# Kernel tuning notes

Measured on AMD Instinct MI355X. Metric: run time of the kernel, lower is better.

Reference implementation:

```python
import jax, jax.numpy as jnp
import numpy as np

PAD = 1
ORDERS = ['back', 'down', 'front', 'left', 'right', 'top']
# connected face for each of ['up','down','left','right'] sides (from self.relation)
NEIGHBORS = {
    'back':  ['top', 'down', 'right', 'left'],
    'down':  ['front', 'back', 'left', 'right'],
    'front': ['top', 'down', 'left', 'right'],
    'left':  ['top', 'down', 'back', 'front'],
    'right': ['top', 'down', 'front', 'back'],
    'top':   ['back', 'front', 'left', 'right'],
}
SIDES = ['up', 'down', 'left', 'right']

def _rot_y(t):
    c, s = np.cos(t), np.sin(t)
    return np.array([[c, 0, s], [0, 1, 0], [-s, 0, c]], np.float64)

def _rot_x(t):
    c, s = np.cos(t), np.sin(t)
    return np.array([[1, 0, 0], [0, c, -s], [0, s, c]], np.float64)

def _precompute(h, pad):
    # Reconstruction of Equirec2Cube geometry used by SpherePad._GetLoc.
    # Padded cube face has side Wp = h + 2*pad and FOV theta = 2*arctan((0.5h+pad)/(0.5h)).
    Wp = h + 2 * pad
    cxp = (Wp - 1) / 2.0
    tan_half = (0.5 * h + pad) / (0.5 * h)  # tan(theta/2)
    fp = cxp / tan_half                      # focal of padded cube (pixel-edge convention)
    u = (np.arange(Wp) - cxp) / fp
    gx, gy = np.meshgrid(u, u)              # x right, y down, camera looks along +z
    grid = np.stack([gx, gy, np.ones_like(gx)], axis=-1)  # [Wp, Wp, 3] front-face rays
    # world->camera rotations per face, ordered/named to match ORDERS
    R = {'back': _rot_y(np.pi), 'down': _rot_x(np.pi / 2), 'front': np.eye(3),
         'left': _rot_y(np.pi / 2), 'right': _rot_y(-np.pi / 2), 'top': _rot_x(-np.pi / 2)}
    data = {}
    for face in ORDERS:
        data[face] = {}
        for j, side in enumerate(SIDES):
            conn = NEIGHBORS[face][j]
            Rrel = R[conn] @ R[face].T       # self-cam -> connected-cam
            g = grid @ Rrel.T                # [Wp, Wp, 3]
            # original FOV=90 K has f == cx, so normalized grid_sample coord = X/Z, Y/Z
            x = g[..., 0] / g[..., 2]
            y = g[..., 1] / g[..., 2]
            mask = (x >= -1.01) & (x <= 1.01) & (y >= -1.01) & (y <= 1.01)
            xy = np.clip(np.stack([x, y], axis=-1), -1.0, 1.0).astype(np.float32)
            if side == 'up':
                sl = (slice(0, pad), slice(None))
            elif side == 'down':
                sl = (slice(Wp - pad, Wp), slice(None))
            elif side == 'left':
                sl = (slice(None), slice(0, pad))
            else:
                sl = (slice(None), slice(Wp - pad, Wp))
            data[face][side] = (xy[sl], mask[sl])
    return data

def _grid_sample(img, grid):
    # img [N,C,H,W], grid [N,Hg,Wg,2] in [-1,1]; bilinear, align_corners=True
    N, C, H, W = img.shape
    x = (grid[..., 0] + 1.0) * 0.5 * (W - 1)
    y = (grid[..., 1] + 1.0) * 0.5 * (H - 1)
    x0 = jnp.floor(x)
    y0 = jnp.floor(y)
    wx = (x - x0)[..., None]
    wy = (y - y0)[..., None]
    x0i = jnp.clip(x0.astype(jnp.int32), 0, W - 1)
    x1i = jnp.clip(x0i + 1, 0, W - 1)
    y0i = jnp.clip(y0.astype(jnp.int32), 0, H - 1)
    y1i = jnp.clip(y0i + 1, 0, H - 1)
    b = jnp.arange(N)[:, None, None]
    v00 = img[b, :, y0i, x0i]  # [N,Hg,Wg,C]
    v01 = img[b, :, y0i, x1i]
    v10 = img[b, :, y1i, x0i]
    v11 = img[b, :, y1i, x1i]
    out = (v00 * (1 - wx) * (1 - wy) + v01 * wx * (1 - wy)
           + v10 * (1 - wx) * wy + v11 * wx * wy)
    return out.transpose(0, 3, 1, 2)  # [N,C,Hg,Wg]

def _forward(inputs, pad):
    bs, c, h, w = inputs.shape
    rep = bs // 6
    data = _precompute(h, pad)       # numpy constants, computed at trace time
    faces = inputs.reshape(rep, 6, c, h, w)   # inputs[i::6] == faces[:, i]
    outs = []
    for i, face in enumerate(ORDERS):
        tf = jnp.pad(faces[:, i], ((0, 0), (0, 0), (pad, pad), (pad, pad)))
        for j, side in enumerate(SIDES):
            conn = faces[:, ORDERS.index(NEIGHBORS[face][j])]
            xy, mask = data[face][side]
            grid = jnp.broadcast_to(jnp.asarray(xy), (rep,) + xy.shape)
            interp = _grid_sample(conn, grid)          # [rep,c,strip_h,strip_w]
            m = jnp.asarray(mask)[None, None]
            if side == 'up':
                tf = tf.at[:, :, :pad, :].set(jnp.where(m, interp, tf[:, :, :pad, :]))
            elif side == 'down':
                tf = tf.at[:, :, -pad:, :].set(jnp.where(m, interp, tf[:, :, -pad:, :]))
            elif side == 'left':
                tf = tf.at[:, :, :, :pad].set(jnp.where(m, interp, tf[:, :, :, :pad]))
            else:
                tf = tf.at[:, :, :, -pad:].set(jnp.where(m, interp, tf[:, :, :, -pad:]))
        outs.append(tf)
    # torch: cat by face then re-interleave -> out[k*6+i] = face i of panorama k
    return jnp.stack(outs, axis=1).reshape(bs, c, h + 2 * pad, w + 2 * pad)

def setup_inputs() -> dict:
    key = jax.random.key(0)
    inputs = jax.random.normal(key, (24, 256, 128, 128), dtype=jnp.float32)
    return {'inputs': inputs}

def reference(inputs):
    return _forward(inputs, PAD)
```

## Files before the change

### kernel.cpp

```cpp
#include <hip/hip_runtime.h>

#define H    128
#define WP   130
#define BPF  516
#define TBLN 3096
#define SPI  1536

__constant__ int c_R[6][9] = {
  {-1,0,0,  0,1,0,  0,0,-1},
  { 1,0,0,  0,0,-1, 0,1,0 },
  { 1,0,0,  0,1,0,  0,0,1 },
  { 0,0,1,  0,1,0, -1,0,0 },
  { 0,0,-1, 0,1,0,  1,0,0 },
  { 1,0,0,  0,0,1,  0,-1,0},
};
__constant__ int c_conn[6][4] = {
  {5,1,4,3}, {2,0,3,4}, {5,1,3,4}, {5,1,0,2}, {5,1,2,0}, {0,2,3,4},
};

#define INV_FP (65.0f / 4128.0f)

__device__ __forceinline__ int stage_index(int y, int x) {
  if (x <= 3)   return 512 + y * 8 + x;
  if (x >= 124) return 512 + y * 8 + 4 + (x - 124);
  int slot = (y == 0) ? 0 : (y == 1) ? 1 : (y == 126) ? 2 : 3;
  return slot * 128 + x;
}

__global__ void __launch_bounds__(256)
border_table_kernel(int* __restrict__ tb_face, int4* __restrict__ tb_raw,
                    int4* __restrict__ tb_stg, float4* __restrict__ tb_w) {
  int t = blockIdx.x * 256 + threadIdx.x;
  if (t >= TBLN) return;
  int face = t / BPF;
  int k    = t - face * BPF;

  int r, c;
  if (k < 130)      { r = 0;        c = k; }
  else if (k < 260) { r = WP - 1;   c = k - 130; }
  else if (k < 388) { r = k - 259;  c = 0; }
  else              { r = k - 387;  c = WP - 1; }

  int fs = -1;
  int4  raw = make_int4(0, 0, 0, 0);
  int4  stg = make_int4(0, 0, 0, 0);
  float4 w  = make_float4(0.f, 0.f, 0.f, 0.f);

  int cand[2]; int nc = 0;
  if (c == WP - 1) cand[nc++] = 3;
  if (c == 0)      cand[nc++] = 2;
  if (r == WP - 1) cand[nc++] = 1;
  if (r == 0)      cand[nc++] = 0;

  float uc = ((float)c - 64.5f) * INV_FP;
  float ur = ((float)r - 64.5f) * INV_FP;

  for (int kk = 0; kk < nc; ++kk) {
    int s  = cand[kk];
    int cf = c_conn[face][s];
    const int* Rc = c_R[cf];
    const int* Rf = c_R[face];
    float g[3];
    #pragma unroll
    for (int i = 0; i < 3; ++i) {
      float acc = 0.0f;
      #pragma unroll
      for (int j = 0; j < 3; ++j) {
        int rr = Rc[i*3+0]*Rf[j*3+0] + Rc[i*3+1]*Rf[j*3+1] + Rc[i*3+2]*Rf[j*3+2];
        float dj = (j == 0) ? uc : (j == 1) ? ur : 1.0f;
        acc += (float)rr * dj;
      }
      g[i] = acc;
    }
    float x = g[0] / g[2];
    float y = g[1] / g[2];
    if (fabsf(x) <= 1.01f && fabsf(y) <= 1.01f) {
      x = fminf(fmaxf(x, -1.0f), 1.0f);
      y = fminf(fmaxf(y, -1.0f), 1.0f);
      float xp = (x + 1.0f) * 0.5f * (float)(H - 1);
      float yp = (y + 1.0f) * 0.5f * (float)(H - 1);
      float x0 = floorf(xp), y0 = floorf(yp);
      float wx = xp - x0,    wy = yp - y0;
      int x0i = min(max((int)x0, 0), H - 1);
      int x1i = min(x0i + 1, H - 1);
      int y0i = min(max((int)y0, 0), H - 1);
      int y1i = min(y0i + 1, H - 1);
      fs  = cf;
      raw = make_int4(y0i * H + x0i, y0i * H + x1i, y1i * H + x0i, y1i * H + x1i);
      stg = make_int4(stage_index(y0i, x0i), stage_index(y0i, x1i),
                      stage_index(y1i, x0i), stage_index(y1i, x1i));
      w   = make_float4((1.f - wx) * (1.f - wy), wx * (1.f - wy),
                        (1.f - wx) * wy,         wx * wy);
      break;
    }
  }
  tb_face[t] = fs;
  tb_raw[t]  = raw;
  tb_stg[t]  = stg;
  tb_w[t]    = w;
}

__global__ void __launch_bounds__(256)
bulk_stage_kernel(const float* __restrict__ in, float4* __restrict__ out4,
                  float* __restrict__ stage) {
  const unsigned bx  = blockIdx.x;
  const unsigned img = blockIdx.y;
  const unsigned u   = threadIdx.x;

  unsigned hh = (bx << 3) + (u >> 5);
  unsigned l  = u & 31u;
  unsigned g  = hh + 1u;
  unsigned m  = g >> 1;
  unsigned h  = g & 1u;

  const float4* base = (const float4*)in + ((size_t)img << 12);
  float4 A = base[(hh << 5) + l];
  float bx0 = __shfl_down(A.x, 1, 32);
  float by0 = __shfl_down(A.y, 1, 32);
  float bz0 = __shfl_down(A.z, 1, 32);

  float4 o = h ? make_float4(A.y, A.z, A.w, bx0)
               : make_float4(A.w, bx0, by0, bz0);
  if (l < 31u)
    out4[(size_t)img * 4225u + 65u * m + 1u + (h << 5) + l] = o;

  float* simg = stage + (size_t)img * SPI;
  if (l == 0u)  *(float4*)(simg + 512u + hh * 8u)      = A;
  if (l == 31u) *(float4*)(simg + 512u + hh * 8u + 4u) = A;
  if (hh == 0u || hh == 1u || hh == 126u || hh == 127u) {
    unsigned slot = (hh == 0u) ? 0u : (hh == 1u) ? 1u : (hh == 126u) ? 2u : 3u;
    *(float4*)(simg + slot * 128u + (l << 2)) = A;
  }
}

__global__ void __launch_bounds__(256)
edge_stage_kernel(float4* __restrict__ out4, const float* __restrict__ stage,
                  const int* __restrict__ tb_face,
                  const int4* __restrict__ tb_stg,
                  const float4* __restrict__ tb_w) {
  const unsigned img = blockIdx.x;
  const unsigned u   = threadIdx.x;

  unsigned n    = img >> 8;
  unsigned ch   = img & 255u;
  unsigned rep  = n / 6u;
  unsigned face = n - rep * 6u;
  const float* simg = stage + (size_t)img * SPI;

  for (unsigned k = u; k < 257u; k += 256u) {
    unsigned qk;
    if (k < 33u)       qk = k;
    else if (k == 33u) qk = 64u;
    else if (k == 34u) qk = 4160u;
    else if (k < 68u)  qk = 4192u + (k - 35u);
    else {
      unsigned jj = k - 68u;
      unsigned mm = 1u + jj / 3u;
      unsigned w  = jj - 3u * (jj / 3u);
      qk = 65u * mm + ((w == 0u) ? 0u : (w == 1u) ? 32u : 64u);
    }

    unsigned p = qk << 2;
    unsigned r = p / 130u;
    unsigned c = p - r * 130u;
    float vals[4];
    #pragma unroll
    for (int jj = 0; jj < 4; ++jj) {
      float v;
      if ((r - 1u) < 128u && (c - 1u) < 128u) {
        unsigned cc = c - 1u;
        unsigned cs = (cc < 4u) ? cc : (cc - 120u);
        v = simg[512u + (r - 1u) * 8u + cs];
      } else {
        unsigned tk = (r == 0u)   ? c
                    : (r == 129u) ? (130u + c)
                    : (c == 0u)   ? (259u + r)
                    :               (387u + r);
        unsigned ti = face * (unsigned)BPF + tk;
        int fs = tb_face[ti];
        v = 0.0f;
        if (fs >= 0) {
          int4   id = tb_stg[ti];
          float4 w  = tb_w[ti];
          const float* sj = stage +
              (size_t)(((rep * 6u + (unsigned)fs) << 8) + ch) * SPI;
          v = w.x * sj[id.x] + w.y * sj[id.y] + w.z * sj[id.z] + w.w * sj[id.w];
        }
      }
      vals[jj] = v;
      if (++c == 130u) { c = 0u; ++r; }
    }
    out4[(size_t)img * 4225u + qk] =
        make_float4(vals[0], vals[1], vals[2], vals[3]);
  }
}

__global__ void __launch_bounds__(256)
fused_kernel(const float* __restrict__ in, float4* __restrict__ out4,
             const int* __restrict__ tb_face,
             const int4* __restrict__ tb_idx,
             const float4* __restrict__ tb_w) {
  const unsigned bx  = blockIdx.x;
  const unsigned img = blockIdx.y;
  const unsigned u   = threadIdx.x;

  if (bx < 16u) {
    unsigned hh = (bx << 3) + (u >> 5);
    unsigned l  = u & 31u;
    unsigned g  = hh + 1u;
    unsigned m  = g >> 1;
    unsigned h  = g & 1u;

    const float4* base = (const float4*)in + ((size_t)img << 12);
    float4 A = base[(hh << 5) + l];
    float bx0 = __shfl_down(A.x, 1, 32);
    float by0 = __shfl_down(A.y, 1, 32);
    float bz0 = __shfl_down(A.z, 1, 32);

    float4 o = h ? make_float4(A.y, A.z, A.w, bx0)
                 : make_float4(A.w, bx0, by0, bz0);
    if (l < 31u)
      out4[(size_t)img * 4225u + 65u * m + 1u + (h << 5) + l] = o;
  } else {
    unsigned n    = img >> 8;
    unsigned ch   = img & 255u;
    unsigned rep  = n / 6u;
    unsigned face = n - rep * 6u;

    for (unsigned k = u; k < 257u; k += 256u) {
      unsigned qk;
      if (k < 33u)       qk = k;
      else if (k == 33u) qk = 64u;
      else if (k == 34u) qk = 4160u;
      else if (k < 68u)  qk = 4192u + (k - 35u);
      else {
        unsigned jj = k - 68u;
        unsigned mm = 1u + jj / 3u;
        unsigned w  = jj - 3u * (jj / 3u);
        qk = 65u * mm + ((w == 0u) ? 0u : (w == 1u) ? 32u : 64u);
      }

      unsigned p = qk << 2;
      unsigned r = p / 130u;
      unsigned c = p - r * 130u;
      float vals[4];
      #pragma unroll
      for (int jj = 0; jj < 4; ++jj) {
        float v;
        if ((r - 1u) < 128u && (c - 1u) < 128u) {
          v = in[(img << 14) + ((r - 1u) << 7) + (c - 1u)];
        } else {
          unsigned tk = (r == 0u)   ? c
                      : (r == 129u) ? (130u + c)
                      : (c == 0u)   ? (259u + r)
                      :               (387u + r);
          unsigned ti = face * (unsigned)BPF + tk;
          int fs = tb_face[ti];
          v = 0.0f;
          if (fs >= 0) {
            int4   id = tb_idx[ti];
            float4 w  = tb_w[ti];
            const float* s = in +
                ((size_t)(((rep * 6u + (unsigned)fs) << 8) + ch) << 14);
            v = w.x * s[id.x] + w.y * s[id.y] + w.z * s[id.z] + w.w * s[id.w];
          }
        }
        vals[jj] = v;
        if (++c == 130u) { c = 0u; ++r; }
      }
      out4[(size_t)img * 4225u + qk] =
          make_float4(vals[0], vals[1], vals[2], vals[3]);
    }
  }
}

__global__ void __launch_bounds__(256)
interior_kernel(const float4* __restrict__ in4, float* __restrict__ out) {
  unsigned t = blockIdx.x * 256u + threadIdx.x;
  unsigned c4  = t & 31u;
  unsigned r   = (t >> 5) & 127u;
  unsigned img = t >> 12;
  float4 v = in4[t];
  unsigned o = img * 16900u + (r + 1u) * 130u + 1u + (c4 << 2);
  out[o] = v.x; out[o + 1] = v.y; out[o + 2] = v.z; out[o + 3] = v.w;
}

__global__ void __launch_bounds__(256)
border_kernel(const float* __restrict__ in, float* __restrict__ out) {
  unsigned tid = blockIdx.x * 256u + threadIdx.x;
  const unsigned total = 6144u * 516u;
  if (tid >= total) return;
  unsigned img = tid / 516u;
  unsigned k   = tid - img * 516u;
  int r, c;
  if (k < 130u)      { r = 0;               c = (int)k; }
  else if (k < 260u) { r = WP - 1;          c = (int)(k - 130u); }
  else if (k < 388u) { r = (int)(k - 259u); c = 0; }
  else               { r = (int)(k - 387u); c = WP - 1; }
  int n = (int)(img >> 8), ch = (int)(img & 255u);
  int face = n % 6, rep = n / 6;
  float v = 0.0f;
  int cand[2]; int nc = 0;
  if (c == WP - 1) cand[nc++] = 3;
  if (c == 0)      cand[nc++] = 2;
  if (r == WP - 1) cand[nc++] = 1;
  if (r == 0)      cand[nc++] = 0;
  float uc = ((float)c - 64.5f) * INV_FP;
  float ur = ((float)r - 64.5f) * INV_FP;
  for (int kk = 0; kk < nc; ++kk) {
    int s = cand[kk], cf = c_conn[face][s];
    const int* Rc = c_R[cf]; const int* Rf = c_R[face];
    float g[3];
    #pragma unroll
    for (int i = 0; i < 3; ++i) {
      float acc = 0.0f;
      #pragma unroll
      for (int j = 0; j < 3; ++j) {
        int rr = Rc[i*3+0]*Rf[j*3+0] + Rc[i*3+1]*Rf[j*3+1] + Rc[i*3+2]*Rf[j*3+2];
        float dj = (j == 0) ? uc : (j == 1) ? ur : 1.0f;
        acc += (float)rr * dj;
      }
      g[i] = acc;
    }
    float x = g[0] / g[2], y = g[1] / g[2];
    if (fabsf(x) <= 1.01f && fabsf(y) <= 1.01f) {
      x = fminf(fmaxf(x, -1.0f), 1.0f);
      y = fminf(fmaxf(y, -1.0f), 1.0f);
      const float* src = in + ((size_t)((rep * 6 + cf) * 256 + ch)) * H * H;
      float xp = (x + 1.0f) * 0.5f * (float)(H - 1);
      float yp = (y + 1.0f) * 0.5f * (float)(H - 1);
      float x0 = floorf(xp), y0 = floorf(yp);
      float wx = xp - x0, wy = yp - y0;
      int x0i = min(max((int)x0, 0), H - 1);
      int x1i = min(x0i + 1, H - 1);
      int y0i = min(max((int)y0, 0), H - 1);
      int y1i = min(y0i + 1, H - 1);
      v = src[y0i*H+x0i]*(1.f-wx)*(1.f-wy) + src[y0i*H+x1i]*wx*(1.f-wy)
        + src[y1i*H+x0i]*(1.f-wx)*wy       + src[y1i*H+x1i]*wx*wy;
      break;
    }
  }
  out[(unsigned)img * 16900u + (unsigned)r * 130u + (unsigned)c] = v;
}

extern "C" void kernel_launch(void* const* d_in, const int* in_sizes, int n_in,
                              void* d_out, int out_size, void* d_ws, size_t ws_size,
                              hipStream_t stream) {
  (void)in_sizes; (void)n_in; (void)out_size;
  const float* in = (const float*)d_in[0];
  float* out = (float*)d_out;

  const size_t tbl_bytes  = (size_t)TBLN * (4 + 16 + 16 + 16);
  const size_t need_full  = tbl_bytes + (size_t)6144 * SPI * 4;

  if (d_ws != nullptr && ws_size >= tbl_bytes) {
    int*    tb_face = (int*)d_ws;
    int4*   tb_raw  = (int4*)(tb_face + TBLN);
    int4*   tb_stg  = tb_raw + TBLN;
    float4* tb_w    = (float4*)(tb_stg + TBLN);
    border_table_kernel<<<(TBLN + 255) / 256, 256, 0, stream>>>(
        tb_face, tb_raw, tb_stg, tb_w);

    if (ws_size >= need_full) {
      float* stage = (float*)(tb_w + TBLN);
      dim3 gridB(16, 6144);
      bulk_stage_kernel<<<gridB, 256, 0, stream>>>(in, (float4*)out, stage);
      edge_stage_kernel<<<6144, 256, 0, stream>>>((float4*)out, stage,
                                                  tb_face, tb_stg, tb_w);
    } else {
      dim3 grid(17, 6144);
      fused_kernel<<<grid, 256, 0, stream>>>(in, (float4*)out,
                                             tb_face, tb_raw, tb_w);
    }
  } else {
    interior_kernel<<<98304, 256, 0, stream>>>((const float4*)in, out);
    const unsigned btotal = 6144u * 516u;
    border_kernel<<<(btotal + 255u) / 256u, 256, 0, stream>>>(in, out);
  }
}
```

Measured before the change: 248.0 us.

## Use persistent wave-per-output-row-pair bulk kernel with fully aligned float4 stores

The bulk copy kernel becomes a persistent grid of 1024 blocks. Each 64-lane wave handles one pair of input rows that maps onto one aligned 65-float4 output segment, so every output float4 store is written whole and aligned. The first and last input rows are left to the edge kernel, which now writes complete top and bottom output rows. The change aims to cut partial, misaligned writes and the block-launch overhead of the 16x6144 grid. The cost is more lane-select logic and a grid-stride loop.

```diff
diff --git a/kernel.cpp b/kernel.cpp
--- a/kernel.cpp
+++ b/kernel.cpp
@@ -5,6 +5,8 @@
 #define BPF  516
 #define TBLN 3096
 #define SPI  1536
+#define NIMG 6144
+#define NT_BULK (6144u * 63u)
 
 __constant__ int c_R[6][9] = {
   {-1,0,0,  0,1,0,  0,0,-1},
@@ -101,60 +103,72 @@
 }
 
 __global__ void __launch_bounds__(256)
-bulk_stage_kernel(const float* __restrict__ in, float4* __restrict__ out4,
-                  float* __restrict__ stage) {
-  const unsigned bx  = blockIdx.x;
-  const unsigned img = blockIdx.y;
-  const unsigned u   = threadIdx.x;
-
-  unsigned hh = (bx << 3) + (u >> 5);
-  unsigned l  = u & 31u;
-  unsigned g  = hh + 1u;
-  unsigned m  = g >> 1;
-  unsigned h  = g & 1u;
-
-  const float4* base = (const float4*)in + ((size_t)img << 12);
-  float4 A = base[(hh << 5) + l];
-  float bx0 = __shfl_down(A.x, 1, 32);
-  float by0 = __shfl_down(A.y, 1, 32);
-  float bz0 = __shfl_down(A.z, 1, 32);
-
-  float4 o = h ? make_float4(A.y, A.z, A.w, bx0)
-               : make_float4(A.w, bx0, by0, bz0);
-  if (l < 31u)
-    out4[(size_t)img * 4225u + 65u * m + 1u + (h << 5) + l] = o;
-
-  float* simg = stage + (size_t)img * SPI;
-  if (l == 0u)  *(float4*)(simg + 512u + hh * 8u)      = A;
-  if (l == 31u) *(float4*)(simg + 512u + hh * 8u + 4u) = A;
-  if (hh == 0u || hh == 1u || hh == 126u || hh == 127u) {
-    unsigned slot = (hh == 0u) ? 0u : (hh == 1u) ? 1u : (hh == 126u) ? 2u : 3u;
-    *(float4*)(simg + slot * 128u + (l << 2)) = A;
-  }
-}
-
-__global__ void __launch_bounds__(256)
-edge_stage_kernel(float4* __restrict__ out4, const float* __restrict__ stage,
-                  const int* __restrict__ tb_face,
-                  const int4* __restrict__ tb_stg,
-                  const float4* __restrict__ tb_w) {
+bulk2_kernel(const float4* __restrict__ in4, float4* __restrict__ out4,
+             float* __restrict__ stage) {
+  const unsigned nwaves = gridDim.x << 2;
+  const unsigned wid = (blockIdx.x << 2) + (threadIdx.x >> 6);
+  const unsigned l   = threadIdx.x & 63u;
+
+  for (unsigned t = wid; t < NT_BULK; t += nwaves) {
+    unsigned img = t / 63u;
+    unsigned m   = t - img * 63u + 1u;
+    const float4* bin = in4 + ((size_t)img << 12);
+    float4 A = bin[(((m << 1) - 1u) << 5) + l];
+
+    float* simg = stage + (size_t)img * SPI;
+    unsigned row = (m << 1) - 1u + (l >> 5);
+    if ((l & 31u) == 0u)  *(float4*)(simg + 512u + row * 8u)      = A;
+    if ((l & 31u) == 31u) *(float4*)(simg + 512u + row * 8u + 4u) = A;
+    if (row == 1u   && l <  32u) *(float4*)(simg + 128u + (l << 2)) = A;
+    if (row == 126u && l >= 32u) *(float4*)(simg + 256u + ((l - 32u) << 2)) = A;
+    if (m == 1u && l < 32u) {
+      float4 E = bin[l];
+      *(float4*)(simg + (l << 2)) = E;
+      if (l == 0u)  *(float4*)(simg + 512u) = E;
+      if (l == 31u) *(float4*)(simg + 512u + 4u) = E;
+    }
+    if (m == 63u && l >= 32u) {
+      unsigned l2 = l - 32u;
+      float4 E = bin[(127u << 5) + l2];
+      *(float4*)(simg + 384u + (l2 << 2)) = E;
+      if (l2 == 0u)  *(float4*)(simg + 512u + 127u * 8u) = E;
+      if (l2 == 31u) *(float4*)(simg + 512u + 127u * 8u + 4u) = E;
+    }
+
+    float pw = __shfl_up(A.w, 1, 64);
+    float py = __shfl_up(A.y, 1, 64);
+    float pz = __shfl_up(A.z, 1, 64);
+
+    float4 o;
+    o.x = (l == 0u)  ? 0.0f : ((l <= 32u) ? pw : py);
+    o.y = (l <= 31u) ? A.x  : ((l == 32u) ? 0.0f : pz);
+    o.z = (l <= 31u) ? A.y  : ((l == 32u) ? 0.0f : pw);
+    o.w = (l <= 31u) ? A.z  : A.x;
+
+    size_t ob = (size_t)img * 4225u + 65u * (size_t)m;
+    out4[ob + l] = o;
+    if (l == 63u) out4[ob + 64u] = make_float4(A.y, A.z, A.w, 0.0f);
+  }
+}
+
+__global__ void __launch_bounds__(256)
+edge2_kernel(float4* __restrict__ out4, const float* __restrict__ stage,
+             const int* __restrict__ tb_face,
+             const int4* __restrict__ tb_stg,
+             const float4* __restrict__ tb_w) {
   const unsigned img = blockIdx.x;
-  const unsigned u   = threadIdx.x;
-
   unsigned n    = img >> 8;
   unsigned ch   = img & 255u;
   unsigned rep  = n / 6u;
   unsigned face = n - rep * 6u;
   const float* simg = stage + (size_t)img * SPI;
 
-  for (unsigned k = u; k < 257u; k += 256u) {
+  for (unsigned j = threadIdx.x; j < 319u; j += 256u) {
     unsigned qk;
-    if (k < 33u)       qk = k;
-    else if (k == 33u) qk = 64u;
-    else if (k == 34u) qk = 4160u;
-    else if (k < 68u)  qk = 4192u + (k - 35u);
+    if (j < 65u)       qk = j;
+    else if (j < 130u) qk = 4160u + (j - 65u);
     else {
-      unsigned jj = k - 68u;
+      unsigned jj = j - 130u;
       unsigned mm = 1u + jj / 3u;
       unsigned w  = jj - 3u * (jj / 3u);
       qk = 65u * mm + ((w == 0u) ? 0u : (w == 1u) ? 32u : 64u);
@@ -165,12 +179,10 @@
     unsigned c = p - r * 130u;
     float vals[4];
     #pragma unroll
-    for (int jj = 0; jj < 4; ++jj) {
+    for (int e = 0; e < 4; ++e) {
       float v;
-      if ((r - 1u) < 128u && (c - 1u) < 128u) {
-        unsigned cc = c - 1u;
-        unsigned cs = (cc < 4u) ? cc : (cc - 120u);
-        v = simg[512u + (r - 1u) * 8u + cs];
+      if (r != 0u && r != 129u && c != 0u && c != 129u) {
+        v = simg[stage_index((int)(r - 1u), (int)(c - 1u))];
       } else {
         unsigned tk = (r == 0u)   ? c
                     : (r == 129u) ? (130u + c)
@@ -187,7 +199,7 @@
           v = w.x * sj[id.x] + w.y * sj[id.y] + w.z * sj[id.z] + w.w * sj[id.w];
         }
       }
-      vals[jj] = v;
+      vals[e] = v;
       if (++c == 130u) { c = 0u; ++r; }
     }
     out4[(size_t)img * 4225u + qk] =
@@ -350,8 +362,8 @@
   const float* in = (const float*)d_in[0];
   float* out = (float*)d_out;
 
-  const size_t tbl_bytes  = (size_t)TBLN * (4 + 16 + 16 + 16);
-  const size_t need_full  = tbl_bytes + (size_t)6144 * SPI * 4;
+  const size_t tbl_bytes = (size_t)TBLN * (4 + 16 + 16 + 16);
+  const size_t need_full = tbl_bytes + (size_t)NIMG * SPI * 4;
 
   if (d_ws != nullptr && ws_size >= tbl_bytes) {
     int*    tb_face = (int*)d_ws;
@@ -363,12 +375,12 @@
 
     if (ws_size >= need_full) {
       float* stage = (float*)(tb_w + TBLN);
-      dim3 gridB(16, 6144);
-      bulk_stage_kernel<<<gridB, 256, 0, stream>>>(in, (float4*)out, stage);
-      edge_stage_kernel<<<6144, 256, 0, stream>>>((float4*)out, stage,
-                                                  tb_face, tb_stg, tb_w);
+      bulk2_kernel<<<1024, 256, 0, stream>>>((const float4*)in,
+                                             (float4*)out, stage);
+      edge2_kernel<<<NIMG, 256, 0, stream>>>((float4*)out, stage,
+                                             tb_face, tb_stg, tb_w);
     } else {
-      dim3 grid(17, 6144);
+      dim3 grid(17, NIMG);
       fused_kernel<<<grid, 256, 0, stream>>>(in, (float4*)out,
                                              tb_face, tb_raw, tb_w);
     }
```

Measured after the change: 251.3 us. About the same (+1.4%).
